# Optimization experiments

Measured on AMD Instinct MI355X. Metric: run time of the kernel, lower is better.

The kernel has to match this reference:

```python
import jax, jax.numpy as jnp
import numpy as np
from jax import lax

DN = ('NCHW', 'OIHW', 'NCHW')


def setup_inputs() -> dict:
    key = jax.random.key(0)
    k1, k2, k3 = jax.random.split(key, 3)
    x = jax.random.normal(k1, (8, 16, 256, 256), dtype=jnp.float32)
    w_perceive = jax.random.normal(k2, (128, 16, 3, 3), dtype=jnp.float32) * 0.02
    w_update = jax.random.normal(k3, (16, 128, 1, 1), dtype=jnp.float32) * 0.01
    return {"x": x, "w_perceive": w_perceive, "w_update": w_update, "steps": 64}


def reference(x, w_perceive, w_update, steps):
    def step(h, _):
        # perceive: 3x3 conv, 16 -> 128 channels, SAME padding, no bias
        p = lax.conv_general_dilated(h, w_perceive, (1, 1), 'SAME', dimension_numbers=DN)
        # update: ReLU then 1x1 conv, 128 -> 16 channels, no bias
        dx = lax.conv_general_dilated(jax.nn.relu(p), w_update, (1, 1), 'SAME', dimension_numbers=DN)
        h = h + dx
        # clamp alive channel to [0,1], hidden channels to [-3,3]
        h = jnp.concatenate([
            jnp.clip(h[:, 0:1], 0.0, 1.0),
            jnp.clip(h[:, 1:], -3.0, 3.0),
        ], axis=1)
        return h, None

    x, _ = lax.scan(step, x, None, length=steps)
    return x
```

## Files before the change

### kernel.cpp

```cpp
#include <hip/hip_runtime.h>
#include <hip/hip_bf16.h>

#define NSTEPS 64

typedef __attribute__((ext_vector_type(8))) short bf16x8;
typedef __attribute__((ext_vector_type(4))) float f32x4;

static __device__ __forceinline__ unsigned short f2bf(float v) {
  union { __hip_bfloat16 h; unsigned short u; } cv;
  cv.h = __float2bfloat16(v);
  return cv.u;
}

static __device__ __forceinline__ unsigned int cvtpk_bf16(float lo, float hi) {
  unsigned int d;
  asm("v_cvt_pk_bf16_f32 %0, %1, %2" : "=v"(d) : "v"(lo), "v"(hi));
  return d;
}

__global__ void ca_prep(const float* __restrict__ w1, const float* __restrict__ w2,
                        __hip_bfloat16* __restrict__ fr) {
  int i = blockIdx.x * 256 + threadIdx.x;
  if (i < 20480) {
    int j  = i & 7;
    int l  = (i >> 3) & 63;
    int fi = i >> 9;
    int kc = fi % 5, mb = fi / 5;
    int m  = l & 15;
    int co = ((mb >> 1) << 5) + ((m >> 2) << 3) + ((mb & 1) << 2) + (m & 3);
    int k  = kc * 32 + ((l >> 4) << 3) + j;
    float v = 0.0f;
    if (k < 144) {
      int tap = k >> 4, ci = k & 15;
      v = w1[(co * 16 + ci) * 9 + tap];
    }
    fr[i] = __float2bfloat16(v);
  } else if (i < 22528) {
    int i2  = i - 20480;
    int j   = i2 & 7;
    int l   = (i2 >> 3) & 63;
    int kc2 = i2 >> 9;
    int k2  = kc2 * 32 + ((l >> 4) << 3) + j;
    fr[i] = __float2bfloat16(w2[(l & 15) * 128 + k2]);
  }
}

#define TILE0 16384
#define TILE1 21568

template <bool IN_NCHW, bool OUT_NCHW>
__launch_bounds__(128, 3)
__global__ void ca_step(const float* __restrict__ hin,
                        float* __restrict__ hout,
                        const __hip_bfloat16* __restrict__ fr) {
  __shared__ __align__(16) char smem[26752];
  const int tid  = threadIdx.x;
  const int lane = tid & 63;
  const int w    = tid >> 6;
  const int bid  = blockIdx.x;
  const int b    = bid & 7;
  const int t    = bid >> 3;
  const int ty   = t >> 4;
  const int tx   = t & 15;
  const int Y0   = ty << 4, X0 = tx << 4;
  const int ib   = b << 20;

  bf16x8 w2f[4];
#pragma unroll
  for (int kc = 0; kc < 4; ++kc)
    w2f[kc] = *(const bf16x8*)(fr + 20480 + ((kc * 64 + lane) << 3));
#pragma unroll
  for (int kc = 0; kc < 4; ++kc)
    asm volatile("" : "+v"(w2f[kc]));

  for (int i = tid; i < 18 * 18; i += 128) {
    int y  = i / 18;
    int x  = i - y * 18;
    int GY = Y0 + y - 1, GX = X0 + x - 1;
    bool inb = ((unsigned)GY < 256u) && ((unsigned)GX < 256u);
    unsigned int pk[8];
    if (IN_NCHW) {
      int gof = ib + (GY << 8) + GX;
#pragma unroll
      for (int c = 0; c < 8; ++c) {
        float v0 = inb ? hin[gof + ((2 * c) << 16)] : 0.0f;
        float v1 = inb ? hin[gof + ((2 * c + 1) << 16)] : 0.0f;
        pk[c] = (unsigned int)f2bf(v0) | ((unsigned int)f2bf(v1) << 16);
      }
    } else {
      f32x4 q[4];
      if (inb) {
        const f32x4* rp = (const f32x4*)(hin + ib + (GY << 12) + (GX << 4));
#pragma unroll
        for (int qq = 0; qq < 4; ++qq) q[qq] = rp[qq];
      } else {
        const f32x4 z = {0.0f, 0.0f, 0.0f, 0.0f};
#pragma unroll
        for (int qq = 0; qq < 4; ++qq) q[qq] = z;
      }
#pragma unroll
      for (int c = 0; c < 8; ++c)
        pk[c] = (unsigned int)f2bf(q[c >> 1][(c & 1) * 2]) |
                ((unsigned int)f2bf(q[c >> 1][(c & 1) * 2 + 1]) << 16);
    }
    *(uint4*)(smem + TILE0 + i * 16) = make_uint4(pk[0], pk[1], pk[2], pk[3]);
    *(uint4*)(smem + TILE1 + i * 16) = make_uint4(pk[4], pk[5], pk[6], pk[7]);
  }
  __syncthreads();

  const int pix     = lane & 15;
  const int g       = lane >> 4;
  const int g1b     = g >> 1;
  const int halfoff = (g & 1) ? TILE1 : TILE0;

  const f32x4 z4 = {0.0f, 0.0f, 0.0f, 0.0f};

#pragma unroll 1
  for (int j = 0; j < 8; ++j) {
    const int bufoff = (j & 1) << 13;

    const int py = Y0 + 2 * j + w;
    float hv[4];
    int gbB_nchw = 0, gbB_nhwc = 0;
    if (IN_NCHW) {
      gbB_nchw = ib + (py << 8) + X0 + pix;
#pragma unroll
      for (int r = 0; r < 4; ++r)
        hv[r] = hin[gbB_nchw + (((g << 2) + r) << 16)];
    } else {
      gbB_nhwc = ib + (py << 12) + ((X0 + pix) << 4) + (g << 2);
      const f32x4 hvv = *(const f32x4*)(hin + gbB_nhwc);
#pragma unroll
      for (int r = 0; r < 4; ++r) hv[r] = hvv[r];
    }

    f32x4 acc[2][4];
#pragma unroll
    for (int i = 0; i < 2; ++i)
#pragma unroll
      for (int ml = 0; ml < 4; ++ml) acc[i][ml] = z4;

#pragma unroll
    for (int kc = 0; kc < 5; ++kc) {
      bf16x8 a1c[4];
#pragma unroll
      for (int ml = 0; ml < 4; ++ml) {
        const int mb = (w << 2) + ml;
        a1c[ml] = *(const bf16x8*)(fr + (((mb * 5 + kc) * 64 + lane) << 3));
      }
      const int t0   = 2 * kc;
      const int t1   = (2 * kc + 1 > 8) ? 8 : 2 * kc + 1;
      const int off0 = ((t0 / 3) * 18 + (t0 % 3)) * 16;
      const int off1 = ((t1 / 3) * 18 + (t1 % 3)) * 16;
#pragma unroll
      for (int i = 0; i < 2; ++i) {
        const char* rowbase = smem + halfoff + ((2 * j + i) * 18 + pix) * 16;
        const bf16x8 b1 = *(const bf16x8*)(rowbase + (g1b ? off1 : off0));
#pragma unroll
        for (int ml = 0; ml < 4; ++ml)
          acc[i][ml] = __builtin_amdgcn_mfma_f32_16x16x32_bf16(a1c[ml], b1,
                                                               acc[i][ml], 0, 0, 0);
      }
    }

#pragma unroll
    for (int i = 0; i < 2; ++i) {
#pragma unroll
      for (int q = 0; q < 2; ++q) {
        const int me = 2 * q, mo = 2 * q + 1;
        union { unsigned int u[4]; bf16x8 v; } bb;
        bb.u[0] = cvtpk_bf16(fmaxf(acc[i][me][0], 0.0f), fmaxf(acc[i][me][1], 0.0f));
        bb.u[1] = cvtpk_bf16(fmaxf(acc[i][me][2], 0.0f), fmaxf(acc[i][me][3], 0.0f));
        bb.u[2] = cvtpk_bf16(fmaxf(acc[i][mo][0], 0.0f), fmaxf(acc[i][mo][1], 0.0f));
        bb.u[3] = cvtpk_bf16(fmaxf(acc[i][mo][2], 0.0f), fmaxf(acc[i][mo][3], 0.0f));
        *(bf16x8*)(smem + bufoff + (i << 12) + (((w << 1) + q) << 10) +
                   (lane << 4)) = bb.v;
      }
    }
    __syncthreads();

    f32x4 dxa = z4;
    const char* bs = smem + bufoff + (w << 12) + (lane << 4);
#pragma unroll
    for (int kc2 = 0; kc2 < 4; ++kc2) {
      const bf16x8 b2 = *(const bf16x8*)(bs + (kc2 << 10));
      dxa = __builtin_amdgcn_mfma_f32_16x16x32_bf16(w2f[kc2], b2, dxa, 0, 0, 0);
    }

    if (OUT_NCHW) {
      const int gbo = ib + (py << 8) + X0 + pix;
#pragma unroll
      for (int r = 0; r < 4; ++r) {
        const int co2 = (g << 2) + r;
        float v = hv[r] + dxa[r];
        const float lo = (co2 == 0) ? 0.0f : -3.0f;
        const float hi = (co2 == 0) ? 1.0f : 3.0f;
        v = fminf(fmaxf(v, lo), hi);
        hout[gbo + (co2 << 16)] = v;
      }
    } else {
      const int gbo = ib + (py << 12) + ((X0 + pix) << 4) + (g << 2);
      f32x4 ov;
#pragma unroll
      for (int r = 0; r < 4; ++r) {
        const int co2 = (g << 2) + r;
        float v = hv[r] + dxa[r];
        const float lo = (co2 == 0) ? 0.0f : -3.0f;
        const float hi = (co2 == 0) ? 1.0f : 3.0f;
        ov[r] = fminf(fmaxf(v, lo), hi);
      }
      *(f32x4*)(hout + gbo) = ov;
    }
  }
}

extern "C" void kernel_launch(void* const* d_in, const int* in_sizes, int n_in,
                              void* d_out, int out_size, void* d_ws, size_t ws_size,
                              hipStream_t stream) {
  const float* x  = (const float*)d_in[0];
  const float* w1 = (const float*)d_in[1];
  const float* w2 = (const float*)d_in[2];
  float* out  = (float*)d_out;
  float* ping = (float*)d_ws;
  __hip_bfloat16* fr = (__hip_bfloat16*)((char*)d_ws + 33554432);

  ca_prep<<<88, 256, 0, stream>>>(w1, w2, fr);

  for (int s = 0; s < NSTEPS; ++s) {
    const float* in = (s == 0) ? x : ((s & 1) ? ping : out);
    float* o        = (s & 1) ? out : ping;
    if (s == 0)
      ca_step<true, false><<<2048, 128, 0, stream>>>(in, o, fr);
    else if (s == NSTEPS - 1)
      ca_step<false, true><<<2048, 128, 0, stream>>>(in, o, fr);
    else
      ca_step<false, false><<<2048, 128, 0, stream>>>(in, o, fr);
  }
}
```

Before: 1.946 ms.

## Process four rows per iteration to reuse weight fragments; use packed bf16 convert

The main loop now covers four tile rows per iteration instead of two, so each weight fragment loaded for the 3x3 conv feeds twice as many MFMAs and the loop runs half as many times. The smem staging buffer is no longer double-buffered, so a second barrier is added at the end of each iteration. Input packing now uses the packed v_cvt_pk_bf16_f32 instruction instead of two scalar conversions. In exchange the accumulator count doubles, which raises register pressure and may hurt occupancy at the 3-blocks launch bound.

```diff
diff --git a/kernel.cpp b/kernel.cpp
--- a/kernel.cpp
+++ b/kernel.cpp
@@ -5,12 +5,6 @@
 
 typedef __attribute__((ext_vector_type(8))) short bf16x8;
 typedef __attribute__((ext_vector_type(4))) float f32x4;
-
-static __device__ __forceinline__ unsigned short f2bf(float v) {
-  union { __hip_bfloat16 h; unsigned short u; } cv;
-  cv.h = __float2bfloat16(v);
-  return cv.u;
-}
 
 static __device__ __forceinline__ unsigned int cvtpk_bf16(float lo, float hi) {
   unsigned int d;
@@ -85,7 +79,7 @@
       for (int c = 0; c < 8; ++c) {
         float v0 = inb ? hin[gof + ((2 * c) << 16)] : 0.0f;
         float v1 = inb ? hin[gof + ((2 * c + 1) << 16)] : 0.0f;
-        pk[c] = (unsigned int)f2bf(v0) | ((unsigned int)f2bf(v1) << 16);
+        pk[c] = cvtpk_bf16(v0, v1);
       }
     } else {
       f32x4 q[4];
@@ -100,8 +94,7 @@
       }
 #pragma unroll
       for (int c = 0; c < 8; ++c)
-        pk[c] = (unsigned int)f2bf(q[c >> 1][(c & 1) * 2]) |
-                ((unsigned int)f2bf(q[c >> 1][(c & 1) * 2 + 1]) << 16);
+        pk[c] = cvtpk_bf16(q[c >> 1][(c & 1) * 2], q[c >> 1][(c & 1) * 2 + 1]);
     }
     *(uint4*)(smem + TILE0 + i * 16) = make_uint4(pk[0], pk[1], pk[2], pk[3]);
     *(uint4*)(smem + TILE1 + i * 16) = make_uint4(pk[4], pk[5], pk[6], pk[7]);
@@ -116,27 +109,27 @@
   const f32x4 z4 = {0.0f, 0.0f, 0.0f, 0.0f};
 
 #pragma unroll 1
-  for (int j = 0; j < 8; ++j) {
-    const int bufoff = (j & 1) << 13;
-
-    const int py = Y0 + 2 * j + w;
-    float hv[4];
-    int gbB_nchw = 0, gbB_nhwc = 0;
-    if (IN_NCHW) {
-      gbB_nchw = ib + (py << 8) + X0 + pix;
-#pragma unroll
-      for (int r = 0; r < 4; ++r)
-        hv[r] = hin[gbB_nchw + (((g << 2) + r) << 16)];
-    } else {
-      gbB_nhwc = ib + (py << 12) + ((X0 + pix) << 4) + (g << 2);
-      const f32x4 hvv = *(const f32x4*)(hin + gbB_nhwc);
-#pragma unroll
-      for (int r = 0; r < 4; ++r) hv[r] = hvv[r];
-    }
-
-    f32x4 acc[2][4];
-#pragma unroll
-    for (int i = 0; i < 2; ++i)
+  for (int J = 0; J < 4; ++J) {
+    float hv[2][4];
+#pragma unroll
+    for (int rr = 0; rr < 2; ++rr) {
+      const int py = Y0 + 4 * J + 2 * w + rr;
+      if (IN_NCHW) {
+        const int gbB = ib + (py << 8) + X0 + pix;
+#pragma unroll
+        for (int r = 0; r < 4; ++r)
+          hv[rr][r] = hin[gbB + (((g << 2) + r) << 16)];
+      } else {
+        const f32x4 hvv =
+            *(const f32x4*)(hin + ib + (py << 12) + ((X0 + pix) << 4) + (g << 2));
+#pragma unroll
+        for (int r = 0; r < 4; ++r) hv[rr][r] = hvv[r];
+      }
+    }
+
+    f32x4 acc[4][4];
+#pragma unroll
+    for (int i = 0; i < 4; ++i)
 #pragma unroll
       for (int ml = 0; ml < 4; ++ml) acc[i][ml] = z4;
 
@@ -153,8 +146,8 @@
       const int off0 = ((t0 / 3) * 18 + (t0 % 3)) * 16;
       const int off1 = ((t1 / 3) * 18 + (t1 % 3)) * 16;
 #pragma unroll
-      for (int i = 0; i < 2; ++i) {
-        const char* rowbase = smem + halfoff + ((2 * j + i) * 18 + pix) * 16;
+      for (int i = 0; i < 4; ++i) {
+        const char* rowbase = smem + halfoff + ((4 * J + i) * 18 + pix) * 16;
         const bf16x8 b1 = *(const bf16x8*)(rowbase + (g1b ? off1 : off0));
 #pragma unroll
         for (int ml = 0; ml < 4; ++ml)
@@ -164,7 +157,7 @@
     }
 
 #pragma unroll
-    for (int i = 0; i < 2; ++i) {
+    for (int i = 0; i < 4; ++i) {
 #pragma unroll
       for (int q = 0; q < 2; ++q) {
         const int me = 2 * q, mo = 2 * q + 1;
@@ -173,44 +166,48 @@
         bb.u[1] = cvtpk_bf16(fmaxf(acc[i][me][2], 0.0f), fmaxf(acc[i][me][3], 0.0f));
         bb.u[2] = cvtpk_bf16(fmaxf(acc[i][mo][0], 0.0f), fmaxf(acc[i][mo][1], 0.0f));
         bb.u[3] = cvtpk_bf16(fmaxf(acc[i][mo][2], 0.0f), fmaxf(acc[i][mo][3], 0.0f));
-        *(bf16x8*)(smem + bufoff + (i << 12) + (((w << 1) + q) << 10) +
-                   (lane << 4)) = bb.v;
+        *(bf16x8*)(smem + (i << 12) + (((w << 1) + q) << 10) + (lane << 4)) = bb.v;
       }
     }
     __syncthreads();
 
-    f32x4 dxa = z4;
-    const char* bs = smem + bufoff + (w << 12) + (lane << 4);
-#pragma unroll
-    for (int kc2 = 0; kc2 < 4; ++kc2) {
-      const bf16x8 b2 = *(const bf16x8*)(bs + (kc2 << 10));
-      dxa = __builtin_amdgcn_mfma_f32_16x16x32_bf16(w2f[kc2], b2, dxa, 0, 0, 0);
-    }
-
-    if (OUT_NCHW) {
-      const int gbo = ib + (py << 8) + X0 + pix;
-#pragma unroll
-      for (int r = 0; r < 4; ++r) {
-        const int co2 = (g << 2) + r;
-        float v = hv[r] + dxa[r];
-        const float lo = (co2 == 0) ? 0.0f : -3.0f;
-        const float hi = (co2 == 0) ? 1.0f : 3.0f;
-        v = fminf(fmaxf(v, lo), hi);
-        hout[gbo + (co2 << 16)] = v;
-      }
-    } else {
-      const int gbo = ib + (py << 12) + ((X0 + pix) << 4) + (g << 2);
-      f32x4 ov;
-#pragma unroll
-      for (int r = 0; r < 4; ++r) {
-        const int co2 = (g << 2) + r;
-        float v = hv[r] + dxa[r];
-        const float lo = (co2 == 0) ? 0.0f : -3.0f;
-        const float hi = (co2 == 0) ? 1.0f : 3.0f;
-        ov[r] = fminf(fmaxf(v, lo), hi);
-      }
-      *(f32x4*)(hout + gbo) = ov;
-    }
+#pragma unroll
+    for (int rr = 0; rr < 2; ++rr) {
+      const int i  = 2 * w + rr;
+      const int py = Y0 + 4 * J + i;
+      f32x4 dxa = z4;
+      const char* bs = smem + (i << 12) + (lane << 4);
+#pragma unroll
+      for (int kc2 = 0; kc2 < 4; ++kc2) {
+        const bf16x8 b2 = *(const bf16x8*)(bs + (kc2 << 10));
+        dxa = __builtin_amdgcn_mfma_f32_16x16x32_bf16(w2f[kc2], b2, dxa, 0, 0, 0);
+      }
+
+      if (OUT_NCHW) {
+        const int gbo = ib + (py << 8) + X0 + pix;
+#pragma unroll
+        for (int r = 0; r < 4; ++r) {
+          const int co2 = (g << 2) + r;
+          float v = hv[rr][r] + dxa[r];
+          const float lo = (co2 == 0) ? 0.0f : -3.0f;
+          const float hi = (co2 == 0) ? 1.0f : 3.0f;
+          v = fminf(fmaxf(v, lo), hi);
+          hout[gbo + (co2 << 16)] = v;
+        }
+      } else {
+        f32x4 ov;
+#pragma unroll
+        for (int r = 0; r < 4; ++r) {
+          const int co2 = (g << 2) + r;
+          float v = hv[rr][r] + dxa[r];
+          const float lo = (co2 == 0) ? 0.0f : -3.0f;
+          const float hi = (co2 == 0) ? 1.0f : 3.0f;
+          ov[r] = fminf(fmaxf(v, lo), hi);
+        }
+        *(f32x4*)(hout + ib + (py << 12) + ((X0 + pix) << 4) + (g << 2)) = ov;
+      }
+    }
+    __syncthreads();
   }
 }
 
```

Measured after the change: 2.533 ms. 1.3x slower.
